# Optimization experiments

Hardware: AMD Instinct MI355X
Metric: run time of the kernel (lower is better)

## Reference

```python
import jax, jax.numpy as jnp
import numpy as np
from jax import lax

DIM = 128
HEADS = 4
HEAD_DIM = DIM // HEADS          # 32
SR = 2
BN_EPS = 1e-5


def setup_inputs() -> dict:
    key = jax.random.key(0)
    ks = jax.random.split(key, 16)
    B, N, C = 8, 3136, DIM
    H = W = 56
    Nkv = (H // SR) * (W // SR)  # 784
    s = 0.05
    inp = {
        "x": jax.random.normal(ks[0], (B, N, C), jnp.float32),
        "relative_pos": jax.random.normal(ks[1], (HEADS, N, Nkv), jnp.float32),
        "Wq": jax.random.normal(ks[2], (C, C), jnp.float32) * s,
        "bq": jnp.zeros((C,), jnp.float32),
        "Wk": jax.random.normal(ks[3], (C, C), jnp.float32) * s,
        "bk": jnp.zeros((C,), jnp.float32),
        "Wv": jax.random.normal(ks[4], (C, C), jnp.float32) * s,
        "bv": jnp.zeros((C,), jnp.float32),
        "conv_w": jax.random.normal(ks[5], (C, 1, SR, SR), jnp.float32) * s,  # depthwise OIHW
        "conv_b": jnp.zeros((C,), jnp.float32),
        "bn_gamma": jnp.ones((C,), jnp.float32),
        "bn_beta": jnp.zeros((C,), jnp.float32),
        "bn_mean": jax.random.normal(ks[6], (C,), jnp.float32) * 0.1,
        "bn_var": jax.random.uniform(ks[7], (C,), jnp.float32, 0.5, 1.5),
        "Wp": jax.random.normal(ks[8], (C, C), jnp.float32) * s,
        "bp": jnp.zeros((C,), jnp.float32),
        "H": H,
        "W": W,
    }
    return inp


def reference(x, relative_pos, Wq, bq, Wk, bk, Wv, bv, conv_w, conv_b,
              bn_gamma, bn_beta, bn_mean, bn_var, Wp, bp, H, W):
    B, N, C = x.shape
    scale = HEAD_DIM ** -0.5

    # q: (B, heads, N, head_dim)
    q = (x @ Wq + bq).reshape(B, N, HEADS, HEAD_DIM).transpose(0, 2, 1, 3)

    # spatial reduction: depthwise conv stride SR + BatchNorm (eval, running stats)
    x_img = x.transpose(0, 2, 1).reshape(B, C, H, W)
    y = lax.conv_general_dilated(
        x_img, conv_w, window_strides=(SR, SR), padding="VALID",
        feature_group_count=C,
        dimension_numbers=("NCHW", "OIHW", "NCHW")) + conv_b[None, :, None, None]
    inv = bn_gamma * lax.rsqrt(bn_var + BN_EPS)
    y = y * inv[None, :, None, None] + (bn_beta - bn_mean * inv)[None, :, None, None]
    x_ = y.reshape(B, C, -1).transpose(0, 2, 1)  # (B, Nkv, C)
    Nkv = x_.shape[1]

    k = (x_ @ Wk + bk).reshape(B, Nkv, HEADS, HEAD_DIM).transpose(0, 2, 1, 3)
    v = (x_ @ Wv + bv).reshape(B, Nkv, HEADS, HEAD_DIM).transpose(0, 2, 1, 3)

    attn = jnp.einsum("bhnd,bhmd->bhnm", q, k) * scale + relative_pos[None]
    attn = jax.nn.softmax(attn, axis=-1)
    out = jnp.einsum("bhnm,bhmd->bhnd", attn, v)
    out = out.transpose(0, 2, 1, 3).reshape(B, N, C)
    return out @ Wp + bp
```

## Files before the change

### kernel.cpp

```cpp
#include <hip/hip_runtime.h>
#include <hip/hip_bf16.h>

#define BATCH 8
#define NQ 3136
#define CDIM 128
#define NHEAD 4
#define HD 32
#define NKV 784
#define HIMG 56
#define SCALE 0.17677669529663687f

typedef __attribute__((ext_vector_type(8))) short bf8_t;
typedef __attribute__((ext_vector_type(4))) float f4_t;

using bf16 = __hip_bfloat16;
using u16  = unsigned short;

static __device__ __forceinline__ float b2f(bf16 v){ return __bfloat162float(v); }
static __device__ __forceinline__ bf16  f2b(float v){ return __float2bfloat16(v); }
static __device__ __forceinline__ short f2s(float v){
  union { bf16 b; short s; } u; u.b = f2b(v); return u.s;
}
static __device__ __forceinline__ float u16f(u16 x){
  union { u16 u; bf16 b; } c; c.u = x; return b2f(c.b);
}
static __device__ __forceinline__ float ld1(const void* p, size_t i, int f){
  return f ? b2f(((const bf16*)p)[i]) : ((const float*)p)[i];
}
static __device__ __forceinline__ float4 ld4f(const void* p, size_t i, int f){
  if (f){
    ushort4 u = *(const ushort4*)((const bf16*)p + i);
    return make_float4(u16f(u.x), u16f(u.y), u16f(u.z), u16f(u.w));
  }
  return *(const float4*)((const float*)p + i);
}
static __device__ __forceinline__ bf8_t ld8(const void* p, size_t i, int f){
  if (f) return *(const bf8_t*)((const bf16*)p + i);
  const float* fp = (const float*)p + i;
  float4 a = *(const float4*)fp;
  float4 b = *(const float4*)(fp + 4);
  bf8_t r;
  r[0]=f2s(a.x); r[1]=f2s(a.y); r[2]=f2s(a.z); r[3]=f2s(a.w);
  r[4]=f2s(b.x); r[5]=f2s(b.y); r[6]=f2s(b.z); r[7]=f2s(b.w);
  return r;
}
static __device__ __forceinline__ int detect_flag(const void* var_raw){
  const u16* h = (const u16*)var_raw;
  int lane = threadIdx.x & 63;
  bool ok = true;
  #pragma unroll
  for (int t = 0; t < 2; t++){
    union { u16 u; bf16 b; } cv; cv.u = h[lane + 64*t];
    float v = b2f(cv.b);
    ok = ok && (v > 0.3f) && (v < 1.7f);
  }
  return (__ballot(ok) == ~0ull) ? 1 : 0;
}

static __device__ __forceinline__ void mfma_row(
    const bf8_t a[4], const bf16* __restrict__ Wt, int m, int g, f4_t acc[8])
{
  #pragma unroll
  for (int ct = 0; ct < 8; ct++){
    f4_t c = {0.f,0.f,0.f,0.f};
    const bf16* bp = Wt + (size_t)(ct*16 + m)*CDIM + 8*g;
    #pragma unroll
    for (int ks = 0; ks < 4; ks++){
      bf8_t b = *(const bf8_t*)(bp + 32*ks);
      c = __builtin_amdgcn_mfma_f32_16x16x32_bf16(a[ks], b, c, 0,0,0);
    }
    acc[ct] = c;
  }
}

__global__ __launch_bounds__(256) void prep_kernel(
    const void* __restrict__ Wq, const void* __restrict__ Wk,
    const void* __restrict__ Wv, const void* __restrict__ Wp,
    const void* __restrict__ var, const void* __restrict__ cw,
    const void* __restrict__ cb, const void* __restrict__ gam,
    const void* __restrict__ bet, const void* __restrict__ mea,
    const void* __restrict__ bq, const void* __restrict__ bk,
    const void* __restrict__ bv, const void* __restrict__ bp,
    bf16* __restrict__ Wqt, bf16* __restrict__ Wkt,
    bf16* __restrict__ Wvt, bf16* __restrict__ Wpt,
    bf16* __restrict__ bqs, bf16* __restrict__ bks,
    bf16* __restrict__ bvs, bf16* __restrict__ bps,
    float* __restrict__ cwf, float* __restrict__ inv, float* __restrict__ shift2)
{
  int f = detect_flag(var);
  int idx = blockIdx.x*256 + threadIdx.x;
  int mat = idx >> 14;
  int e   = idx & 16383;
  int o = e >> 7, i = e & 127;
  const void* src; bf16* dst; float s = 1.f;
  if      (mat == 0){ src = Wq; dst = Wqt; s = SCALE; }
  else if (mat == 1){ src = Wk; dst = Wkt; }
  else if (mat == 2){ src = Wv; dst = Wvt; }
  else              { src = Wp; dst = Wpt; }
  dst[e] = f2b(ld1(src, (size_t)i*128 + o, f) * s);

  if (blockIdx.x == 0){
    int t = threadIdx.x;
    { int e2 = t;       cwf[(e2&3)*128 + (e2>>2)] = ld1(cw, e2, f); }
    { int e2 = t + 256; cwf[(e2&3)*128 + (e2>>2)] = ld1(cw, e2, f); }
    if (t < 128){
      bqs[t] = f2b(ld1(bq, t, f) * SCALE);
      bks[t] = f2b(ld1(bk, t, f));
      bvs[t] = f2b(ld1(bv, t, f));
      bps[t] = f2b(ld1(bp, t, f));
      float iv = ld1(gam, t, f) * rsqrtf(ld1(var, t, f) + 1e-5f);
      inv[t] = iv;
      shift2[t] = ld1(bet, t, f) - ld1(mea, t, f) * iv + ld1(cb, t, f) * iv;
    }
  }
}

__global__ __launch_bounds__(256) void kvconv_kernel(
    const void* __restrict__ x, const void* __restrict__ var,
    const float* __restrict__ cwf, const float* __restrict__ inv,
    const float* __restrict__ shift2,
    const bf16* __restrict__ Wkt, const bf16* __restrict__ Wvt,
    const bf16* __restrict__ bks, const bf16* __restrict__ bvs,
    bf16* __restrict__ kbf, bf16* __restrict__ vtb)
{
  int f = detect_flag(var);
  __shared__ bf16 xl[64*136];
  int row0 = blockIdx.x*64;

  #pragma unroll
  for (int it = 0; it < 8; it++){
    int s  = it*256 + threadIdx.x;
    int lr = s >> 5;
    int c0 = (s & 31)*4;
    int t  = row0 + lr;
    int b  = t / NKV;
    int kv = t - b*NKV;
    int i = kv/28, j = kv - i*28;
    size_t base = (size_t)(b*NQ + 2*i*HIMG + 2*j)*CDIM + c0;
    float4 t0 = ld4f(x, base, f);
    float4 t1 = ld4f(x, base + CDIM, f);
    float4 t2 = ld4f(x, base + HIMG*CDIM, f);
    float4 t3 = ld4f(x, base + HIMG*CDIM + CDIM, f);
    float4 w0 = *(const float4*)(cwf + c0);
    float4 w1 = *(const float4*)(cwf + 128 + c0);
    float4 w2 = *(const float4*)(cwf + 256 + c0);
    float4 w3 = *(const float4*)(cwf + 384 + c0);
    float4 iv4 = *(const float4*)(inv + c0);
    float4 sh4 = *(const float4*)(shift2 + c0);
    union { u16 h[4]; uint2 u; } pk;
    float a;
    a = t0.x*w0.x + t1.x*w1.x + t2.x*w2.x + t3.x*w3.x; pk.h[0] = (u16)f2s(a*iv4.x + sh4.x);
    a = t0.y*w0.y + t1.y*w1.y + t2.y*w2.y + t3.y*w3.y; pk.h[1] = (u16)f2s(a*iv4.y + sh4.y);
    a = t0.z*w0.z + t1.z*w1.z + t2.z*w2.z + t3.z*w3.z; pk.h[2] = (u16)f2s(a*iv4.z + sh4.z);
    a = t0.w*w0.w + t1.w*w1.w + t2.w*w2.w + t3.w*w3.w; pk.h[3] = (u16)f2s(a*iv4.w + sh4.w);
    *(uint2*)(xl + lr*136 + c0) = pk.u;
  }
  __syncthreads();

  int wave = threadIdx.x >> 6, lane = threadIdx.x & 63;
  int m = lane & 15, g = lane >> 4;
  int r16 = wave*16;
  bf8_t a[4];
  #pragma unroll
  for (int ks = 0; ks < 4; ks++)
    a[ks] = *(const bf8_t*)(xl + (r16 + m)*136 + 8*g + 32*ks);
  int grow = row0 + r16;

  {
    f4_t acc[8];
    mfma_row(a, Wkt, m, g, acc);
    #pragma unroll
    for (int ct = 0; ct < 8; ct++){
      int col = ct*16 + m;
      float bv = b2f(bks[col]);
      #pragma unroll
      for (int r = 0; r < 4; r++)
        kbf[(size_t)(grow + 4*g + r)*CDIM + col] = f2b(acc[ct][r] + bv);
    }
  }
  {
    f4_t acc[8];
    mfma_row(a, Wvt, m, g, acc);
    int b2  = grow / NKV;
    int kv0 = grow - b2*NKV + 4*g;
    #pragma unroll
    for (int ct = 0; ct < 8; ct++){
      int col = ct*16 + m;
      float bv = b2f(bvs[col]);
      int h = col >> 5, d = col & 31;
      union { bf16 hh[4]; uint2 u; } pk;
      #pragma unroll
      for (int r = 0; r < 4; r++) pk.hh[r] = f2b(acc[ct][r] + bv);
      *(uint2*)(vtb + (size_t)((b2*NHEAD + h)*HD + d)*NKV + kv0) = pk.u;
    }
  }
}

template<int RM> struct RelV { using T = float4; };
template<> struct RelV<1> { using T = uint2; };

template<int RM>
static __device__ __forceinline__ typename RelV<RM>::T relld(const void* relp, int off){
  if constexpr (RM == 1) return *(const uint2*)((const bf16*)relp + off);
  else                   return *(const float4*)((const float*)relp + off);
}
template<int RM>
static __device__ __forceinline__ float relget(const typename RelV<RM>::T& v, int r){
  if constexpr (RM == 1){
    union { uint2 u; u16 h[4]; } c; c.u = v;
    return u16f(c.h[r]);
  } else {
    return r == 0 ? v.x : (r == 1 ? v.y : (r == 2 ? v.z : v.w));
  }
}
template<int RM>
static __device__ __forceinline__ void ldrel8(
    typename RelV<RM>::T rl[8], const void* relp, int off){
  #pragma unroll
  for (int t = 0; t < 8; t++) rl[t] = relld<RM>(relp, off + 16*t);
}

template<int RM, int PF>
static __device__ __forceinline__ void chunk128(
    int kv0,
    typename RelV<RM>::T rl[8], bf8_t kc[8],
    typename RelV<RM>::T rln[8], bf8_t kn[8],
    const void* __restrict__ relp, const bf16* __restrict__ kbase,
    const bf16* __restrict__ vb0, const bf16* __restrict__ vb1,
    bf16* __restrict__ pl, int m, int g, bf8_t q8,
    float& m_run, float& l_run, f4_t& O0, f4_t& O1)
{
  f4_t s[8];
  #pragma unroll
  for (int t = 0; t < 8; t++){
    f4_t z = {0.f,0.f,0.f,0.f};
    s[t] = __builtin_amdgcn_mfma_f32_16x16x32_bf16(kc[t], q8, z, 0,0,0);
  }
  if constexpr (PF == 2){
    #pragma unroll
    for (int t = 0; t < 8; t++)
      kn[t] = *(const bf8_t*)(kbase + (size_t)(kv0 + 128 + t*16)*CDIM);
  } else if constexpr (PF == 1){
    kn[0] = *(const bf8_t*)(kbase + (size_t)768*CDIM);
  }
  bf8_t v0[4], v1[4];
  #pragma unroll
  for (int ks = 0; ks < 4; ks++){
    v0[ks] = *(const bf8_t*)(vb0 + kv0 + ks*32 + 8*g);
    v1[ks] = *(const bf8_t*)(vb1 + kv0 + ks*32 + 8*g);
  }
  #pragma unroll
  for (int t = 0; t < 8; t++)
    #pragma unroll
    for (int r = 0; r < 4; r++)
      s[t][r] += relget<RM>(rl[t], r);
  if constexpr (PF == 2) ldrel8<RM>(rln, relp, kv0 + 128 + 4*g);
  else if constexpr (PF == 1) rln[0] = relld<RM>(relp, 768 + 4*g);
  float vmax = s[0][0];
  #pragma unroll
  for (int t = 0; t < 8; t++)
    #pragma unroll
    for (int r = 0; r < 4; r++)
      if (t + r > 0) vmax = fmaxf(vmax, s[t][r]);
  vmax = fmaxf(vmax, __shfl_xor(vmax, 16, 64));
  vmax = fmaxf(vmax, __shfl_xor(vmax, 32, 64));
  if (!__all(vmax <= m_run + 8.f)){
    float mn = fmaxf(m_run, vmax);
    float al = __expf(m_run - mn);
    m_run = mn;
    l_run *= al;
    float alT[4];
    #pragma unroll
    for (int r = 0; r < 4; r++) alT[r] = __shfl(al, 4*g + r, 64);
    #pragma unroll
    for (int r = 0; r < 4; r++){ O0[r] *= alT[r]; O1[r] *= alT[r]; }
  }
  float lsum = 0.f;
  #pragma unroll
  for (int t = 0; t < 8; t++){
    union { u16 h[4]; uint2 u; } pk;
    #pragma unroll
    for (int r = 0; r < 4; r++){
      float p = __expf(s[t][r] - m_run);
      lsum += p;
      pk.h[r] = (u16)f2s(p);
    }
    *(uint2*)(pl + m*136 + t*16 + 4*g) = pk.u;
  }
  l_run += lsum;
  #pragma unroll
  for (int ks = 0; ks < 4; ks++){
    bf8_t a8 = *(const bf8_t*)(pl + m*136 + ks*32 + 8*g);
    O0 = __builtin_amdgcn_mfma_f32_16x16x32_bf16(a8, v0[ks], O0, 0,0,0);
    O1 = __builtin_amdgcn_mfma_f32_16x16x32_bf16(a8, v1[ks], O1, 0,0,0);
  }
}

template<int RM>
static __device__ __forceinline__ void attn_run(
    const void* __restrict__ relp, const bf16* __restrict__ kbase,
    const bf16* __restrict__ vb0, const bf16* __restrict__ vb1,
    bf16* __restrict__ pl, int m, int g,
    bf8_t q8, float& m_run, float& l_run, f4_t& O0, f4_t& O1)
{
  using RT = typename RelV<RM>::T;
  RT rlA[8], rlB[8];
  bf8_t kA[8], kB[8];
  ldrel8<RM>(rlA, relp, 4*g);
  #pragma unroll
  for (int t = 0; t < 8; t++)
    kA[t] = *(const bf8_t*)(kbase + (size_t)(t*16)*CDIM);

  chunk128<RM,2>(0,   rlA,kA, rlB,kB, relp,kbase,vb0,vb1,pl,m,g,q8,m_run,l_run,O0,O1);
  chunk128<RM,2>(128, rlB,kB, rlA,kA, relp,kbase,vb0,vb1,pl,m,g,q8,m_run,l_run,O0,O1);
  chunk128<RM,2>(256, rlA,kA, rlB,kB, relp,kbase,vb0,vb1,pl,m,g,q8,m_run,l_run,O0,O1);
  chunk128<RM,2>(384, rlB,kB, rlA,kA, relp,kbase,vb0,vb1,pl,m,g,q8,m_run,l_run,O0,O1);
  chunk128<RM,2>(512, rlA,kA, rlB,kB, relp,kbase,vb0,vb1,pl,m,g,q8,m_run,l_run,O0,O1);
  chunk128<RM,1>(640, rlB,kB, rlA,kA, relp,kbase,vb0,vb1,pl,m,g,q8,m_run,l_run,O0,O1);

  {
    f4_t z = {0.f,0.f,0.f,0.f};
    f4_t s1 = __builtin_amdgcn_mfma_f32_16x16x32_bf16(kA[0], q8, z, 0,0,0);
    #pragma unroll
    for (int r = 0; r < 4; r++) s1[r] += relget<RM>(rlA[0], r);
    float vmax = fmaxf(fmaxf(s1[0], s1[1]), fmaxf(s1[2], s1[3]));
    vmax = fmaxf(vmax, __shfl_xor(vmax, 16, 64));
    vmax = fmaxf(vmax, __shfl_xor(vmax, 32, 64));
    if (!__all(vmax <= m_run + 8.f)){
      float mn = fmaxf(m_run, vmax);
      float al = __expf(m_run - mn);
      m_run = mn;
      l_run *= al;
      float alT[4];
      #pragma unroll
      for (int r = 0; r < 4; r++) alT[r] = __shfl(al, 4*g + r, 64);
      #pragma unroll
      for (int r = 0; r < 4; r++){ O0[r] *= alT[r]; O1[r] *= alT[r]; }
    }
    union { u16 h[4]; uint2 u; } pk;
    float lsum = 0.f;
    #pragma unroll
    for (int r = 0; r < 4; r++){
      float p = __expf(s1[r] - m_run);
      lsum += p;
      pk.h[r] = (u16)f2s(p);
    }
    *(uint2*)(pl + m*136 + 4*g) = pk.u;
    l_run += lsum;
    bf8_t a8, v0, v1;
    if (g >= 2){
      bf8_t z8 = {0,0,0,0,0,0,0,0};
      a8 = z8; v0 = z8; v1 = z8;
    } else {
      a8 = *(const bf8_t*)(pl + m*136 + 8*g);
      v0 = *(const bf8_t*)(vb0 + 768 + 8*g);
      v1 = *(const bf8_t*)(vb1 + 768 + 8*g);
    }
    O0 = __builtin_amdgcn_mfma_f32_16x16x32_bf16(a8, v0, O0, 0,0,0);
    O1 = __builtin_amdgcn_mfma_f32_16x16x32_bf16(a8, v1, O1, 0,0,0);
  }
}

__global__ __launch_bounds__(64) void attn_kernel(
    const void* __restrict__ x,
    const bf16* __restrict__ Wqt, const bf16* __restrict__ bqs,
    const bf16* __restrict__ kb, const bf16* __restrict__ vtb,
    const void* __restrict__ rel, const void* __restrict__ var,
    void* __restrict__ dout, bf16* __restrict__ obf)
{
  int f = detect_flag(var);
  int lane = threadIdx.x & 63;
  int m = lane & 15, g = lane >> 4;
  int qt = blockIdx.x, h = blockIdx.y, b = blockIdx.z;
  int qrow0 = qt*16;

  __shared__ bf16 Plds[16*136];
  bf16* pl = Plds;

  bf8_t q8;
  {
    bf8_t xa[4];
    #pragma unroll
    for (int ks = 0; ks < 4; ks++)
      xa[ks] = ld8(x, (size_t)(b*NQ + qrow0 + m)*CDIM + 8*g + 32*ks, f);
    f4_t qc0 = {0.f,0.f,0.f,0.f}, qc1 = {0.f,0.f,0.f,0.f};
    const bf16* wp0 = Wqt + (size_t)(h*HD + m)*CDIM + 8*g;
    const bf16* wp1 = Wqt + (size_t)(h*HD + 16 + m)*CDIM + 8*g;
    #pragma unroll
    for (int ks = 0; ks < 4; ks++){
      bf8_t w0 = *(const bf8_t*)(wp0 + 32*ks);
      bf8_t w1 = *(const bf8_t*)(wp1 + 32*ks);
      qc0 = __builtin_amdgcn_mfma_f32_16x16x32_bf16(xa[ks], w0, qc0, 0,0,0);
      qc1 = __builtin_amdgcn_mfma_f32_16x16x32_bf16(xa[ks], w1, qc1, 0,0,0);
    }
    float bv0 = b2f(bqs[h*HD + m]);
    float bv1 = b2f(bqs[h*HD + 16 + m]);
    #pragma unroll
    for (int r = 0; r < 4; r++){
      pl[(4*g + r)*136 + m]      = f2b(qc0[r] + bv0);
      pl[(4*g + r)*136 + 16 + m] = f2b(qc1[r] + bv1);
    }
    q8 = *(const bf8_t*)(pl + m*136 + 8*g);
  }

  const bf16* kbase = kb  + (size_t)(b*NKV + m)*CDIM + h*HD + 8*g;
  const bf16* vb0   = vtb + (size_t)((b*NHEAD + h)*HD + m)*NKV;
  const bf16* vb1   = vtb + (size_t)((b*NHEAD + h)*HD + 16 + m)*NKV;
  size_t rrow = ((size_t)h*NQ + qrow0 + m)*(size_t)NKV;

  float m_run = -1e30f, l_run = 0.f;
  f4_t O0 = {0.f,0.f,0.f,0.f}, O1 = {0.f,0.f,0.f,0.f};

  if (f) attn_run<1>((const void*)((const bf16*)rel + rrow), kbase, vb0, vb1,
                     pl, m, g, q8, m_run, l_run, O0, O1);
  else   attn_run<0>((const void*)((const float*)rel + rrow), kbase, vb0, vb1,
                     pl, m, g, q8, m_run, l_run, O0, O1);

  l_run += __shfl_xor(l_run, 16, 64);
  l_run += __shfl_xor(l_run, 32, 64);
  float lT[4];
  #pragma unroll
  for (int r = 0; r < 4; r++) lT[r] = __shfl(l_run, 4*g + r, 64);

  bf16* ob = f ? (bf16*)dout : obf;
  size_t orow = (size_t)(b*NQ + qrow0 + 4*g);
  #pragma unroll
  for (int r = 0; r < 4; r++){
    float iv = 1.0f / lT[r];
    ob[(orow + r)*CDIM + h*HD + m]      = f2b(O0[r] * iv);
    ob[(orow + r)*CDIM + h*HD + 16 + m] = f2b(O1[r] * iv);
  }
}

__global__ __launch_bounds__(256) void proj_kernel(
    const bf16* A0, const bf16* A1, const bf16* __restrict__ Wt,
    const bf16* __restrict__ bias, void* outp, const void* __restrict__ var)
{
  int f = detect_flag(var);
  const bf16* A = f ? A0 : A1;
  int wave = threadIdx.x >> 6, lane = threadIdx.x & 63;
  int m = lane & 15, g = lane >> 4;
  int row0 = (blockIdx.x*4 + wave)*16;
  bf8_t a[4];
  #pragma unroll
  for (int ks = 0; ks < 4; ks++)
    a[ks] = *(const bf8_t*)(A + (size_t)(row0 + m)*CDIM + 8*g + 32*ks);
  f4_t acc[8];
  mfma_row(a, Wt, m, g, acc);
  #pragma unroll
  for (int ct = 0; ct < 8; ct++){
    int col = ct*16 + m;
    float bv = b2f(bias[col]);
    #pragma unroll
    for (int r = 0; r < 4; r++){
      size_t oi = (size_t)(row0 + 4*g + r)*CDIM + col;
      float v = acc[ct][r] + bv;
      if (f) ((bf16*)outp)[oi]  = f2b(v);
      else   ((float*)outp)[oi] = v;
    }
  }
}

extern "C" void kernel_launch(void* const* d_in, const int* in_sizes, int n_in,
                              void* d_out, int out_size, void* d_ws, size_t ws_size,
                              hipStream_t stream)
{
  const void* x   = d_in[0];
  const void* rel = d_in[1];
  const void* Wq  = d_in[2];
  const void* bq  = d_in[3];
  const void* Wk  = d_in[4];
  const void* bk  = d_in[5];
  const void* Wv  = d_in[6];
  const void* bv  = d_in[7];
  const void* cw  = d_in[8];
  const void* cb  = d_in[9];
  const void* gam = d_in[10];
  const void* bet = d_in[11];
  const void* mea = d_in[12];
  const void* var = d_in[13];
  const void* Wp  = d_in[14];
  const void* bp  = d_in[15];

  char* w = (char*)d_ws;
  auto alloc = [&](size_t bytes){
    char* p = w; w += (bytes + 255) & ~(size_t)255; return p;
  };
  bf16* Wqt = (bf16*)alloc(128*128*sizeof(bf16));
  bf16* Wkt = (bf16*)alloc(128*128*sizeof(bf16));
  bf16* Wvt = (bf16*)alloc(128*128*sizeof(bf16));
  bf16* Wpt = (bf16*)alloc(128*128*sizeof(bf16));
  bf16* bqs = (bf16*)alloc(128*sizeof(bf16));
  bf16* bks = (bf16*)alloc(128*sizeof(bf16));
  bf16* bvs = (bf16*)alloc(128*sizeof(bf16));
  bf16* bps = (bf16*)alloc(128*sizeof(bf16));
  float* cwf    = (float*)alloc(512*sizeof(float));
  float* inv    = (float*)alloc(128*sizeof(float));
  float* shift2 = (float*)alloc(128*sizeof(float));
  bf16* kbf = (bf16*)alloc((size_t)BATCH*NKV*CDIM*sizeof(bf16));
  bf16* vtb = (bf16*)alloc((size_t)BATCH*NKV*CDIM*sizeof(bf16));
  bf16* obf = (bf16*)alloc((size_t)BATCH*NQ*CDIM*sizeof(bf16));

  prep_kernel<<<256, 256, 0, stream>>>(Wq, Wk, Wv, Wp, var, cw, cb, gam, bet, mea,
                                       bq, bk, bv, bp,
                                       Wqt, Wkt, Wvt, Wpt, bqs, bks, bvs, bps,
                                       cwf, inv, shift2);
  kvconv_kernel<<<98, 256, 0, stream>>>(x, var, cwf, inv, shift2,
                                        Wkt, Wvt, bks, bvs, kbf, vtb);
  dim3 ag(196, NHEAD, BATCH);
  attn_kernel<<<ag, 64, 0, stream>>>(x, Wqt, bqs, kbf, vtb, rel, var, d_out, obf);
  proj_kernel<<<392, 256, 0, stream>>>((const bf16*)d_out, obf, Wpt, bps, d_out, var);
}
```

Measured before the change: 228.1 us.

## Fuse output projection into attention and pre-convert relative_pos to bf16

The attention kernel now runs four heads per 256-thread block, gathers the normalized head outputs in shared memory and applies the output projection in place, which removes the separate projection kernel and the intermediate output buffer round-trip. The kvconv kernel gains extra blocks that convert the fp32 relative_pos into a bf16 workspace copy, so attention reads half the bytes of the largest input. The K and V projections are split across waves with smaller row tiles. The trade-off is an extra full read and write of relative_pos in the kvconv kernel every call, plus added synchronization inside the attention block.

```diff
diff --git a/kernel.cpp b/kernel.cpp
--- a/kernel.cpp
+++ b/kernel.cpp
@@ -121,78 +121,92 @@
     const float* __restrict__ shift2,
     const bf16* __restrict__ Wkt, const bf16* __restrict__ Wvt,
     const bf16* __restrict__ bks, const bf16* __restrict__ bvs,
-    bf16* __restrict__ kbf, bf16* __restrict__ vtb)
+    bf16* __restrict__ kbf, bf16* __restrict__ vtb,
+    const void* __restrict__ rel, bf16* __restrict__ relb)
 {
   int f = detect_flag(var);
-  __shared__ bf16 xl[64*136];
-  int row0 = blockIdx.x*64;
-
-  #pragma unroll
-  for (int it = 0; it < 8; it++){
-    int s  = it*256 + threadIdx.x;
-    int lr = s >> 5;
-    int c0 = (s & 31)*4;
-    int t  = row0 + lr;
-    int b  = t / NKV;
-    int kv = t - b*NKV;
-    int i = kv/28, j = kv - i*28;
-    size_t base = (size_t)(b*NQ + 2*i*HIMG + 2*j)*CDIM + c0;
-    float4 t0 = ld4f(x, base, f);
-    float4 t1 = ld4f(x, base + CDIM, f);
-    float4 t2 = ld4f(x, base + HIMG*CDIM, f);
-    float4 t3 = ld4f(x, base + HIMG*CDIM + CDIM, f);
-    float4 w0 = *(const float4*)(cwf + c0);
-    float4 w1 = *(const float4*)(cwf + 128 + c0);
-    float4 w2 = *(const float4*)(cwf + 256 + c0);
-    float4 w3 = *(const float4*)(cwf + 384 + c0);
-    float4 iv4 = *(const float4*)(inv + c0);
-    float4 sh4 = *(const float4*)(shift2 + c0);
-    union { u16 h[4]; uint2 u; } pk;
-    float a;
-    a = t0.x*w0.x + t1.x*w1.x + t2.x*w2.x + t3.x*w3.x; pk.h[0] = (u16)f2s(a*iv4.x + sh4.x);
-    a = t0.y*w0.y + t1.y*w1.y + t2.y*w2.y + t3.y*w3.y; pk.h[1] = (u16)f2s(a*iv4.y + sh4.y);
-    a = t0.z*w0.z + t1.z*w1.z + t2.z*w2.z + t3.z*w3.z; pk.h[2] = (u16)f2s(a*iv4.z + sh4.z);
-    a = t0.w*w0.w + t1.w*w1.w + t2.w*w2.w + t3.w*w3.w; pk.h[3] = (u16)f2s(a*iv4.w + sh4.w);
-    *(uint2*)(xl + lr*136 + c0) = pk.u;
-  }
-  __syncthreads();
-
-  int wave = threadIdx.x >> 6, lane = threadIdx.x & 63;
-  int m = lane & 15, g = lane >> 4;
-  int r16 = wave*16;
-  bf8_t a[4];
-  #pragma unroll
-  for (int ks = 0; ks < 4; ks++)
-    a[ks] = *(const bf8_t*)(xl + (r16 + m)*136 + 8*g + 32*ks);
-  int grow = row0 + r16;
-
-  {
-    f4_t acc[8];
-    mfma_row(a, Wkt, m, g, acc);
-    #pragma unroll
-    for (int ct = 0; ct < 8; ct++){
-      int col = ct*16 + m;
-      float bv = b2f(bks[col]);
+  __shared__ bf16 xl[32*136];
+  if (blockIdx.x < 196){
+    int row0 = blockIdx.x*32;
+    #pragma unroll
+    for (int it = 0; it < 4; it++){
+      int s  = it*256 + threadIdx.x;
+      int lr = s >> 5;
+      int c0 = (s & 31)*4;
+      int t  = row0 + lr;
+      int b  = t / NKV;
+      int kv = t - b*NKV;
+      int i = kv/28, j = kv - i*28;
+      size_t base = (size_t)(b*NQ + 2*i*HIMG + 2*j)*CDIM + c0;
+      float4 t0 = ld4f(x, base, f);
+      float4 t1 = ld4f(x, base + CDIM, f);
+      float4 t2 = ld4f(x, base + HIMG*CDIM, f);
+      float4 t3 = ld4f(x, base + HIMG*CDIM + CDIM, f);
+      float4 w0 = *(const float4*)(cwf + c0);
+      float4 w1 = *(const float4*)(cwf + 128 + c0);
+      float4 w2 = *(const float4*)(cwf + 256 + c0);
+      float4 w3 = *(const float4*)(cwf + 384 + c0);
+      float4 iv4 = *(const float4*)(inv + c0);
+      float4 sh4 = *(const float4*)(shift2 + c0);
+      union { u16 h[4]; uint2 u; } pk;
+      float a;
+      a = t0.x*w0.x + t1.x*w1.x + t2.x*w2.x + t3.x*w3.x; pk.h[0] = (u16)f2s(a*iv4.x + sh4.x);
+      a = t0.y*w0.y + t1.y*w1.y + t2.y*w2.y + t3.y*w3.y; pk.h[1] = (u16)f2s(a*iv4.y + sh4.y);
+      a = t0.z*w0.z + t1.z*w1.z + t2.z*w2.z + t3.z*w3.z; pk.h[2] = (u16)f2s(a*iv4.z + sh4.z);
+      a = t0.w*w0.w + t1.w*w1.w + t2.w*w2.w + t3.w*w3.w; pk.h[3] = (u16)f2s(a*iv4.w + sh4.w);
+      *(uint2*)(xl + lr*136 + c0) = pk.u;
+    }
+    __syncthreads();
+
+    int wave = threadIdx.x >> 6, lane = threadIdx.x & 63;
+    int m = lane & 15, g = lane >> 4;
+    int r16 = (wave & 1)*16;
+    bf8_t a[4];
+    #pragma unroll
+    for (int ks = 0; ks < 4; ks++)
+      a[ks] = *(const bf8_t*)(xl + (r16 + m)*136 + 8*g + 32*ks);
+    int grow = row0 + r16;
+
+    if (wave < 2){
+      f4_t acc[8];
+      mfma_row(a, Wkt, m, g, acc);
       #pragma unroll
-      for (int r = 0; r < 4; r++)
-        kbf[(size_t)(grow + 4*g + r)*CDIM + col] = f2b(acc[ct][r] + bv);
-    }
-  }
-  {
-    f4_t acc[8];
-    mfma_row(a, Wvt, m, g, acc);
-    int b2  = grow / NKV;
-    int kv0 = grow - b2*NKV + 4*g;
-    #pragma unroll
-    for (int ct = 0; ct < 8; ct++){
-      int col = ct*16 + m;
-      float bv = b2f(bvs[col]);
-      int h = col >> 5, d = col & 31;
-      union { bf16 hh[4]; uint2 u; } pk;
+      for (int ct = 0; ct < 8; ct++){
+        int col = ct*16 + m;
+        float bv = b2f(bks[col]);
+        #pragma unroll
+        for (int r = 0; r < 4; r++)
+          kbf[(size_t)(grow + 4*g + r)*CDIM + col] = f2b(acc[ct][r] + bv);
+      }
+    } else {
+      f4_t acc[8];
+      mfma_row(a, Wvt, m, g, acc);
+      int b2  = grow / NKV;
+      int kv0 = grow - b2*NKV + 4*g;
       #pragma unroll
-      for (int r = 0; r < 4; r++) pk.hh[r] = f2b(acc[ct][r] + bv);
-      *(uint2*)(vtb + (size_t)((b2*NHEAD + h)*HD + d)*NKV + kv0) = pk.u;
-    }
+      for (int ct = 0; ct < 8; ct++){
+        int col = ct*16 + m;
+        float bv = b2f(bvs[col]);
+        int h = col >> 5, d = col & 31;
+        union { bf16 hh[4]; uint2 u; } pk;
+        #pragma unroll
+        for (int r = 0; r < 4; r++) pk.hh[r] = f2b(acc[ct][r] + bv);
+        *(uint2*)(vtb + (size_t)((b2*NHEAD + h)*HD + d)*NKV + kv0) = pk.u;
+      }
+    }
+  } else {
+    if (f) return;
+    int bi = blockIdx.x - 196;
+    size_t gid = ((size_t)bi*256 + threadIdx.x)*8;
+    const float* fp = (const float*)rel + gid;
+    float4 a  = *(const float4*)fp;
+    float4 b4 = *(const float4*)(fp + 4);
+    union { u16 hh[8]; uint4 u4; } pk;
+    pk.hh[0]=(u16)f2s(a.x);  pk.hh[1]=(u16)f2s(a.y);
+    pk.hh[2]=(u16)f2s(a.z);  pk.hh[3]=(u16)f2s(a.w);
+    pk.hh[4]=(u16)f2s(b4.x); pk.hh[5]=(u16)f2s(b4.y);
+    pk.hh[6]=(u16)f2s(b4.z); pk.hh[7]=(u16)f2s(b4.w);
+    *(uint4*)(relb + gid) = pk.u4;
   }
 }
 
@@ -361,21 +375,25 @@
   }
 }
 
-__global__ __launch_bounds__(64) void attn_kernel(
+template<int FB>
+static __device__ __forceinline__ void attn_device(
     const void* __restrict__ x,
     const bf16* __restrict__ Wqt, const bf16* __restrict__ bqs,
+    const bf16* __restrict__ Wpt, const bf16* __restrict__ bps,
     const bf16* __restrict__ kb, const bf16* __restrict__ vtb,
-    const void* __restrict__ rel, const void* __restrict__ var,
-    void* __restrict__ dout, bf16* __restrict__ obf)
+    const void* __restrict__ rel, const bf16* __restrict__ relb,
+    const void* __restrict__ var, void* __restrict__ dout)
 {
   int f = detect_flag(var);
-  int lane = threadIdx.x & 63;
+  int wave = threadIdx.x >> 6, lane = threadIdx.x & 63;
   int m = lane & 15, g = lane >> 4;
-  int qt = blockIdx.x, h = blockIdx.y, b = blockIdx.z;
+  int qt = blockIdx.x, b = blockIdx.y;
+  if (qt >= 196) return;
+  int h = wave;
   int qrow0 = qt*16;
 
-  __shared__ bf16 Plds[16*136];
-  bf16* pl = Plds;
+  __shared__ bf16 Plds[4][16*136];
+  bf16* pl = Plds[wave];
 
   bf8_t q8;
   {
@@ -411,10 +429,16 @@
   float m_run = -1e30f, l_run = 0.f;
   f4_t O0 = {0.f,0.f,0.f,0.f}, O1 = {0.f,0.f,0.f,0.f};
 
-  if (f) attn_run<1>((const void*)((const bf16*)rel + rrow), kbase, vb0, vb1,
-                     pl, m, g, q8, m_run, l_run, O0, O1);
-  else   attn_run<0>((const void*)((const float*)rel + rrow), kbase, vb0, vb1,
-                     pl, m, g, q8, m_run, l_run, O0, O1);
+  if constexpr (FB == 0){
+    const void* rsrc = f ? (const void*)((const bf16*)rel + rrow)
+                         : (const void*)(relb + rrow);
+    attn_run<1>(rsrc, kbase, vb0, vb1, pl, m, g, q8, m_run, l_run, O0, O1);
+  } else {
+    if (f) attn_run<1>((const void*)((const bf16*)rel + rrow), kbase, vb0, vb1,
+                       pl, m, g, q8, m_run, l_run, O0, O1);
+    else   attn_run<0>((const void*)((const float*)rel + rrow), kbase, vb0, vb1,
+                       pl, m, g, q8, m_run, l_run, O0, O1);
+  }
 
   l_run += __shfl_xor(l_run, 16, 64);
   l_run += __shfl_xor(l_run, 32, 64);
@@ -422,43 +446,62 @@
   #pragma unroll
   for (int r = 0; r < 4; r++) lT[r] = __shfl(l_run, 4*g + r, 64);
 
-  bf16* ob = f ? (bf16*)dout : obf;
-  size_t orow = (size_t)(b*NQ + qrow0 + 4*g);
+  __syncthreads();
+  bf16* Ot = &Plds[0][0];
   #pragma unroll
   for (int r = 0; r < 4; r++){
     float iv = 1.0f / lT[r];
-    ob[(orow + r)*CDIM + h*HD + m]      = f2b(O0[r] * iv);
-    ob[(orow + r)*CDIM + h*HD + 16 + m] = f2b(O1[r] * iv);
-  }
-}
-
-__global__ __launch_bounds__(256) void proj_kernel(
-    const bf16* A0, const bf16* A1, const bf16* __restrict__ Wt,
-    const bf16* __restrict__ bias, void* outp, const void* __restrict__ var)
-{
-  int f = detect_flag(var);
-  const bf16* A = f ? A0 : A1;
-  int wave = threadIdx.x >> 6, lane = threadIdx.x & 63;
-  int m = lane & 15, g = lane >> 4;
-  int row0 = (blockIdx.x*4 + wave)*16;
+    Ot[(4*g + r)*136 + h*HD + m]      = f2b(O0[r] * iv);
+    Ot[(4*g + r)*136 + h*HD + 16 + m] = f2b(O1[r] * iv);
+  }
+  __syncthreads();
+
   bf8_t a[4];
   #pragma unroll
   for (int ks = 0; ks < 4; ks++)
-    a[ks] = *(const bf8_t*)(A + (size_t)(row0 + m)*CDIM + 8*g + 32*ks);
-  f4_t acc[8];
-  mfma_row(a, Wt, m, g, acc);
-  #pragma unroll
-  for (int ct = 0; ct < 8; ct++){
-    int col = ct*16 + m;
-    float bv = b2f(bias[col]);
+    a[ks] = *(const bf8_t*)(Ot + m*136 + 8*g + 32*ks);
+  #pragma unroll
+  for (int cgi = 0; cgi < 2; cgi++){
+    int cg = 2*h + cgi;
+    f4_t c = {0.f,0.f,0.f,0.f};
+    const bf16* bp = Wpt + (size_t)(cg*16 + m)*CDIM + 8*g;
+    #pragma unroll
+    for (int ks = 0; ks < 4; ks++){
+      bf8_t w = *(const bf8_t*)(bp + 32*ks);
+      c = __builtin_amdgcn_mfma_f32_16x16x32_bf16(a[ks], w, c, 0,0,0);
+    }
+    int col = cg*16 + m;
+    float bv = b2f(bps[col]);
     #pragma unroll
     for (int r = 0; r < 4; r++){
-      size_t oi = (size_t)(row0 + 4*g + r)*CDIM + col;
-      float v = acc[ct][r] + bv;
-      if (f) ((bf16*)outp)[oi]  = f2b(v);
-      else   ((float*)outp)[oi] = v;
-    }
-  }
+      size_t oi = (size_t)(b*NQ + qrow0 + 4*g + r)*CDIM + col;
+      float v = c[r] + bv;
+      if (f) ((bf16*)dout)[oi]  = f2b(v);
+      else   ((float*)dout)[oi] = v;
+    }
+  }
+}
+
+__global__ __launch_bounds__(256) void attn_kernel(
+    const void* __restrict__ x,
+    const bf16* __restrict__ Wqt, const bf16* __restrict__ bqs,
+    const bf16* __restrict__ Wpt, const bf16* __restrict__ bps,
+    const bf16* __restrict__ kb, const bf16* __restrict__ vtb,
+    const void* __restrict__ rel, const bf16* __restrict__ relb,
+    const void* __restrict__ var, void* __restrict__ dout)
+{
+  attn_device<0>(x, Wqt, bqs, Wpt, bps, kb, vtb, rel, relb, var, dout);
+}
+
+__global__ __launch_bounds__(256) void attn_kernel_fb(
+    const void* __restrict__ x,
+    const bf16* __restrict__ Wqt, const bf16* __restrict__ bqs,
+    const bf16* __restrict__ Wpt, const bf16* __restrict__ bps,
+    const bf16* __restrict__ kb, const bf16* __restrict__ vtb,
+    const void* __restrict__ rel, const bf16* __restrict__ relb,
+    const void* __restrict__ var, void* __restrict__ dout)
+{
+  attn_device<1>(x, Wqt, bqs, Wpt, bps, kb, vtb, rel, relb, var, dout);
 }
 
 extern "C" void kernel_launch(void* const* d_in, const int* in_sizes, int n_in,
@@ -499,15 +542,25 @@
   float* shift2 = (float*)alloc(128*sizeof(float));
   bf16* kbf = (bf16*)alloc((size_t)BATCH*NKV*CDIM*sizeof(bf16));
   bf16* vtb = (bf16*)alloc((size_t)BATCH*NKV*CDIM*sizeof(bf16));
-  bf16* obf = (bf16*)alloc((size_t)BATCH*NQ*CDIM*sizeof(bf16));
+
+  size_t relb_bytes = (size_t)NHEAD*NQ*NKV*sizeof(bf16);
+  bf16* relb = nullptr;
+  if (((char*)d_ws + ws_size) - w >= (ptrdiff_t)(relb_bytes + 256))
+    relb = (bf16*)alloc(relb_bytes);
+
+  int rblk = relb ? 4802 : 0;
 
   prep_kernel<<<256, 256, 0, stream>>>(Wq, Wk, Wv, Wp, var, cw, cb, gam, bet, mea,
                                        bq, bk, bv, bp,
                                        Wqt, Wkt, Wvt, Wpt, bqs, bks, bvs, bps,
                                        cwf, inv, shift2);
-  kvconv_kernel<<<98, 256, 0, stream>>>(x, var, cwf, inv, shift2,
-                                        Wkt, Wvt, bks, bvs, kbf, vtb);
-  dim3 ag(196, NHEAD, BATCH);
-  attn_kernel<<<ag, 64, 0, stream>>>(x, Wqt, bqs, kbf, vtb, rel, var, d_out, obf);
-  proj_kernel<<<392, 256, 0, stream>>>((const bf16*)d_out, obf, Wpt, bps, d_out, var);
-}
+  kvconv_kernel<<<196 + rblk, 256, 0, stream>>>(
+      x, var, cwf, inv, shift2, Wkt, Wvt, bks, bvs, kbf, vtb, rel, relb);
+  dim3 ag(200, BATCH);
+  if (relb)
+    attn_kernel<<<ag, 256, 0, stream>>>(
+        x, Wqt, bqs, Wpt, bps, kbf, vtb, rel, relb, var, d_out);
+  else
+    attn_kernel_fb<<<ag, 256, 0, stream>>>(
+        x, Wqt, bqs, Wpt, bps, kbf, vtb, rel, relb, var, d_out);
+}
```

New measurement: 212.8 us. 6.7% less time.
